# Kernel optimization log

Measured on AMD Instinct MI355X. Metric: run time of the kernel, lower is better.

## Reference

```python
import jax, jax.numpy as jnp
import numpy as np

VOCAB, HIDDEN, EMBED = 30522, 768, 512
PAD_INDEX = 0
NEG_SLOPE = 0.1


def setup_inputs() -> dict:
    key = jax.random.key(0)
    k1, k2, k3, k4 = jax.random.split(key, 4)
    words = jax.random.randint(k1, (16, 512, 4), 0, VOCAB, dtype=jnp.int64) if jax.config.jax_enable_x64 else jax.random.randint(k1, (16, 512, 4), 0, VOCAB, dtype=jnp.int32)
    embed_table = jax.random.normal(k2, (VOCAB, HIDDEN), dtype=jnp.float32) * 0.02
    w_ffn = jax.random.normal(k3, (HIDDEN, EMBED), dtype=jnp.float32) * 0.02
    b_ffn = jax.random.normal(k4, (EMBED,), dtype=jnp.float32) * 0.02
    return {"words": words, "embed_table": embed_table, "w_ffn": w_ffn, "b_ffn": b_ffn}


def reference(words, embed_table, w_ffn, b_ffn):
    # words: [B, S, W] subword ids; pad_index marks padding subwords/words.
    B, S, W = words.shape
    sub_mask = words != PAD_INDEX                      # [B,S,W] valid subwords
    word_valid = jnp.any(sub_mask, axis=-1)            # [B,S]  words with >=1 subword
    lens = jnp.sum(word_valid, axis=-1)                # [B]    valid words per sequence

    # Stub of transformer last_hidden_state: per-token hidden vectors. [B,S,W,H]
    x = embed_table[words]

    # Masked mean over subwords of each word (segment mean-pool).
    m = sub_mask[..., None].astype(x.dtype)
    cnt = jnp.maximum(jnp.sum(sub_mask, axis=-1), 1)[..., None].astype(x.dtype)
    pooled = jnp.sum(x * m, axis=2) / cnt              # [B,S,H]

    # pad = x[0, -1] of flattened [B, S*W, H] == hidden of last flat token of batch 0
    pad_vec = x[0, -1, -1]                             # [H]

    # Stable compaction: valid words first (mirrors pop-in-order + pad append).
    order = jnp.argsort(jnp.logical_not(word_valid), axis=1, stable=True)  # [B,S]
    pooled_c = jnp.take_along_axis(pooled, order[..., None], axis=1)       # [B,S,H]
    keep = (jnp.arange(S)[None, :] < lens[:, None])[..., None]             # [B,S,1]
    x_seq = jnp.where(keep, pooled_c, pad_vec)         # [B,S,H]

    # FFN: Linear + LeakyReLU(0.1)
    return jax.nn.leaky_relu(x_seq @ w_ffn + b_ffn, NEG_SLOPE)
```

## Files before the change

### kernel.cpp

```cpp
#include <hip/hip_runtime.h>
#include <stdint.h>

#define HIDDEN 768
#define EMBED  512
#define BATCH  16
#define SEQ    512
#define NWORDS (BATCH*SEQ)
#define PAD_FLAT_IDX 2047
#define NEG_SLOPE 0.1f

__device__ __forceinline__ unsigned short f2bf(float f) {
    unsigned int x = __float_as_uint(f);
    unsigned int r = x + 0x7fffu + ((x >> 16) & 1u);
    return (unsigned short)(r >> 16);
}

__global__ __launch_bounds__(512) void scan_kernel(const int* __restrict__ words,
                                                   int* __restrict__ dest) {
    int b = blockIdx.x;
    int s = threadIdx.x;
    int idx = b * SEQ + s;
    int4 w4 = ((const int4*)words)[idx];
    bool valid = (w4.x | w4.y | w4.z | w4.w) != 0;

    unsigned long long m = __ballot(valid);
    int lane = s & 63;
    int wave = s >> 6;
    int wpre = __popcll(m & ((1ull << lane) - 1ull));
    __shared__ int wsum[8];
    if (lane == 0) wsum[wave] = __popcll(m);
    __syncthreads();
    int off = 0, tot = 0;
#pragma unroll
    for (int i = 0; i < 8; ++i) {
        int t = wsum[i];
        if (i < wave) off += t;
        tot += t;
    }
    int vp = off + wpre;
    int d = valid ? vp : (tot + (s - vp));
    dest[idx] = b * SEQ + d;
}

__global__ __launch_bounds__(192) void pool_kernel(const int* __restrict__ words,
                                                   const float* __restrict__ table,
                                                   const int* __restrict__ dest,
                                                   unsigned short* __restrict__ xseq) {
    int word = blockIdx.x;
    int t = threadIdx.x;
    int4 w4 = ((const int4*)words)[word];
    int cnt = (w4.x != 0) + (w4.y != 0) + (w4.z != 0) + (w4.w != 0);

    float ax = 0.f, ay = 0.f, az = 0.f, aw = 0.f;
    if (cnt == 0) {
        int pid = words[PAD_FLAT_IDX];
        float4 v = ((const float4*)(table + (size_t)pid * HIDDEN))[t];
        ax = v.x; ay = v.y; az = v.z; aw = v.w;
    } else {
        if (w4.x != 0) { float4 v = ((const float4*)(table + (size_t)w4.x * HIDDEN))[t]; ax += v.x; ay += v.y; az += v.z; aw += v.w; }
        if (w4.y != 0) { float4 v = ((const float4*)(table + (size_t)w4.y * HIDDEN))[t]; ax += v.x; ay += v.y; az += v.z; aw += v.w; }
        if (w4.z != 0) { float4 v = ((const float4*)(table + (size_t)w4.z * HIDDEN))[t]; ax += v.x; ay += v.y; az += v.z; aw += v.w; }
        if (w4.w != 0) { float4 v = ((const float4*)(table + (size_t)w4.w * HIDDEN))[t]; ax += v.x; ay += v.y; az += v.z; aw += v.w; }
        float inv = 1.0f / (float)cnt;
        ax *= inv; ay *= inv; az *= inv; aw *= inv;
    }
    ushort4 o;
    o.x = f2bf(ax); o.y = f2bf(ay); o.z = f2bf(az); o.w = f2bf(aw);
    int drow = dest[word];
    ((ushort4*)(xseq + (size_t)drow * HIDDEN))[t] = o;
}

__global__ __launch_bounds__(256) void wt_kernel(const float* __restrict__ w,
                                                 unsigned short* __restrict__ wt) {
    __shared__ float tile[32][33];
    int k0 = blockIdx.x * 32;
    int n0 = blockIdx.y * 32;
    int tc = threadIdx.x & 31;
    int tr = threadIdx.x >> 5;
#pragma unroll
    for (int i = 0; i < 4; ++i) {
        int r = tr + i * 8;
        tile[r][tc] = w[(size_t)(k0 + r) * EMBED + n0 + tc];
    }
    __syncthreads();
#pragma unroll
    for (int i = 0; i < 4; ++i) {
        int r = tr + i * 8;
        wt[(size_t)(n0 + r) * HIDDEN + k0 + tc] = f2bf(tile[tc][r]);
    }
}

typedef __attribute__((ext_vector_type(8))) short bf16x8;
typedef __attribute__((ext_vector_type(4))) float f32x4;

__device__ __forceinline__ void load_lds16(const void* g, void* l) {
    __builtin_amdgcn_global_load_lds(
        (const __attribute__((address_space(1))) unsigned int*)g,
        (__attribute__((address_space(3))) unsigned int*)l,
        16, 0, 0);
}

#define BM 64
#define BN 128
#define BK 32

__global__ __launch_bounds__(256) void gemm_kernel(const unsigned short* __restrict__ A,
                                                   const unsigned short* __restrict__ Bt,
                                                   const float* __restrict__ bias,
                                                   float* __restrict__ out) {
    __shared__ unsigned short sA[BM * BK];
    __shared__ unsigned short sB[BN * BK];

    int tid  = threadIdx.x;
    int m0   = blockIdx.x * BM;
    int n0   = blockIdx.y * BN;
    int wave = tid >> 6;
    int lane = tid & 63;
    int wr   = wave >> 1;
    int wc   = wave & 1;
    int quad = lane >> 4;
    int l16  = lane & 15;

    f32x4 acc[2][4] = {};

    int r_s = tid >> 2;
    int k_s = (tid & 3) * 8;

    const unsigned short* ga = A  + (size_t)(m0 + r_s) * HIDDEN + k_s;
    const unsigned short* gb0 = Bt + (size_t)(n0 + r_s) * HIDDEN + k_s;
    const unsigned short* gb1 = Bt + (size_t)(n0 + r_s + 64) * HIDDEN + k_s;

    for (int k0 = 0; k0 < HIDDEN; k0 += BK) {
        load_lds16(ga + k0,  &sA[tid * 8]);
        load_lds16(gb0 + k0, &sB[tid * 8]);
        load_lds16(gb1 + k0, &sB[(256 + tid) * 8]);
        __syncthreads();

        bf16x8 af[2], bf[4];
#pragma unroll
        for (int mt = 0; mt < 2; ++mt)
            af[mt] = *(const bf16x8*)&sA[(wr * 32 + mt * 16 + l16) * BK + quad * 8];
#pragma unroll
        for (int nt = 0; nt < 4; ++nt)
            bf[nt] = *(const bf16x8*)&sB[(wc * 64 + nt * 16 + l16) * BK + quad * 8];

#pragma unroll
        for (int mt = 0; mt < 2; ++mt)
#pragma unroll
            for (int nt = 0; nt < 4; ++nt)
                acc[mt][nt] = __builtin_amdgcn_mfma_f32_16x16x32_bf16(
                    af[mt], bf[nt], acc[mt][nt], 0, 0, 0);
        __syncthreads();
    }

#pragma unroll
    for (int nt = 0; nt < 4; ++nt) {
        int col = n0 + wc * 64 + nt * 16 + l16;
        float bv = bias[col];
#pragma unroll
        for (int mt = 0; mt < 2; ++mt) {
            int rbase = m0 + wr * 32 + mt * 16 + quad * 4;
#pragma unroll
            for (int r = 0; r < 4; ++r) {
                float v = acc[mt][nt][r] + bv;
                v = (v > 0.f) ? v : v * NEG_SLOPE;
                out[(size_t)(rbase + r) * EMBED + col] = v;
            }
        }
    }
}

extern "C" void kernel_launch(void* const* d_in, const int* in_sizes, int n_in,
                              void* d_out, int out_size, void* d_ws, size_t ws_size,
                              hipStream_t stream) {
    (void)in_sizes; (void)n_in; (void)out_size; (void)ws_size;
    const int*   words = (const int*)d_in[0];
    const float* table = (const float*)d_in[1];
    const float* wffn  = (const float*)d_in[2];
    const float* bffn  = (const float*)d_in[3];
    float* out = (float*)d_out;

    char* ws = (char*)d_ws;
    unsigned short* xseq = (unsigned short*)ws;
    unsigned short* wt   = (unsigned short*)(ws + 12582912);
    int*            dest = (int*)(ws + 12582912 + 786432);

    scan_kernel<<<BATCH, SEQ, 0, stream>>>(words, dest);
    wt_kernel<<<dim3(HIDDEN / 32, EMBED / 32), 256, 0, stream>>>(wffn, wt);
    pool_kernel<<<NWORDS, 192, 0, stream>>>(words, table, dest, xseq);
    gemm_kernel<<<dim3(NWORDS / BM, EMBED / BN), 256, 0, stream>>>(xseq, wt, bffn, out);
}
```

Baseline: 165.6 us.

## Merge scan and weight-transpose kernels, reshape GEMM tile to 128x64

Measured after the change: 162.5 us. About the same (-1.9%).

```diff
diff --git a/kernel.cpp b/kernel.cpp
--- a/kernel.cpp
+++ b/kernel.cpp
@@ -15,31 +15,60 @@
     return (unsigned short)(r >> 16);
 }
 
-__global__ __launch_bounds__(512) void scan_kernel(const int* __restrict__ words,
-                                                   int* __restrict__ dest) {
-    int b = blockIdx.x;
-    int s = threadIdx.x;
-    int idx = b * SEQ + s;
-    int4 w4 = ((const int4*)words)[idx];
-    bool valid = (w4.x | w4.y | w4.z | w4.w) != 0;
+__global__ __launch_bounds__(256) void prep_kernel(const int* __restrict__ words,
+                                                   const float* __restrict__ w,
+                                                   int* __restrict__ dest,
+                                                   unsigned short* __restrict__ wt) {
+    if (blockIdx.x < BATCH) {
+        int b = blockIdx.x;
+        int t = threadIdx.x;
+        int s0 = 2 * t, s1 = 2 * t + 1;
+        int4 wa = ((const int4*)words)[b * SEQ + s0];
+        int4 wb = ((const int4*)words)[b * SEQ + s1];
+        bool v0 = (wa.x | wa.y | wa.z | wa.w) != 0;
+        bool v1 = (wb.x | wb.y | wb.z | wb.w) != 0;
 
-    unsigned long long m = __ballot(valid);
-    int lane = s & 63;
-    int wave = s >> 6;
-    int wpre = __popcll(m & ((1ull << lane) - 1ull));
-    __shared__ int wsum[8];
-    if (lane == 0) wsum[wave] = __popcll(m);
-    __syncthreads();
-    int off = 0, tot = 0;
+        unsigned long long m0 = __ballot(v0);
+        unsigned long long m1 = __ballot(v1);
+        int lane = t & 63;
+        int wave = t >> 6;
+        unsigned long long below = (1ull << lane) - 1ull;
+        int pre = __popcll(m0 & below) + __popcll(m1 & below);
+        __shared__ int wsum[4];
+        if (lane == 0) wsum[wave] = __popcll(m0) + __popcll(m1);
+        __syncthreads();
+        int off = 0, tot = 0;
 #pragma unroll
-    for (int i = 0; i < 8; ++i) {
-        int t = wsum[i];
-        if (i < wave) off += t;
-        tot += t;
+        for (int i = 0; i < 4; ++i) {
+            int x = wsum[i];
+            if (i < wave) off += x;
+            tot += x;
+        }
+        int vp0 = off + pre;
+        int vp1 = vp0 + (v0 ? 1 : 0);
+        int d0 = v0 ? vp0 : (tot + (s0 - vp0));
+        int d1 = v1 ? vp1 : (tot + (s1 - vp1));
+        dest[b * SEQ + s0] = b * SEQ + d0;
+        dest[b * SEQ + s1] = b * SEQ + d1;
+    } else {
+        __shared__ float tile[32][33];
+        int bid = blockIdx.x - BATCH;
+        int k0 = (bid % (HIDDEN / 32)) * 32;
+        int n0 = (bid / (HIDDEN / 32)) * 32;
+        int tc = threadIdx.x & 31;
+        int tr = threadIdx.x >> 5;
+#pragma unroll
+        for (int i = 0; i < 4; ++i) {
+            int r = tr + i * 8;
+            tile[r][tc] = w[(size_t)(k0 + r) * EMBED + n0 + tc];
+        }
+        __syncthreads();
+#pragma unroll
+        for (int i = 0; i < 4; ++i) {
+            int r = tr + i * 8;
+            wt[(size_t)(n0 + r) * HIDDEN + k0 + tc] = f2bf(tile[tc][r]);
+        }
     }
-    int vp = off + wpre;
-    int d = valid ? vp : (tot + (s - vp));
-    dest[idx] = b * SEQ + d;
 }
 
 __global__ __launch_bounds__(192) void pool_kernel(const int* __restrict__ words,
@@ -48,6 +77,7 @@
                                                    unsigned short* __restrict__ xseq) {
     int word = blockIdx.x;
     int t = threadIdx.x;
+    int drow = dest[word];
     int4 w4 = ((const int4*)words)[word];
     int cnt = (w4.x != 0) + (w4.y != 0) + (w4.z != 0) + (w4.w != 0);
 
@@ -66,28 +96,7 @@
     }
     ushort4 o;
     o.x = f2bf(ax); o.y = f2bf(ay); o.z = f2bf(az); o.w = f2bf(aw);
-    int drow = dest[word];
     ((ushort4*)(xseq + (size_t)drow * HIDDEN))[t] = o;
-}
-
-__global__ __launch_bounds__(256) void wt_kernel(const float* __restrict__ w,
-                                                 unsigned short* __restrict__ wt) {
-    __shared__ float tile[32][33];
-    int k0 = blockIdx.x * 32;
-    int n0 = blockIdx.y * 32;
-    int tc = threadIdx.x & 31;
-    int tr = threadIdx.x >> 5;
-#pragma unroll
-    for (int i = 0; i < 4; ++i) {
-        int r = tr + i * 8;
-        tile[r][tc] = w[(size_t)(k0 + r) * EMBED + n0 + tc];
-    }
-    __syncthreads();
-#pragma unroll
-    for (int i = 0; i < 4; ++i) {
-        int r = tr + i * 8;
-        wt[(size_t)(n0 + r) * HIDDEN + k0 + tc] = f2bf(tile[tc][r]);
-    }
 }
 
 typedef __attribute__((ext_vector_type(8))) short bf16x8;
@@ -100,8 +109,8 @@
         16, 0, 0);
 }
 
-#define BM 64
-#define BN 128
+#define BM 128
+#define BN 64
 #define BK 32
 
 __global__ __launch_bounds__(256) void gemm_kernel(const unsigned short* __restrict__ A,
@@ -121,45 +130,42 @@
     int quad = lane >> 4;
     int l16  = lane & 15;
 
-    f32x4 acc[2][4] = {};
+    f32x4 acc[4][2] = {};
 
-    int r_s = tid >> 2;
-    int k_s = (tid & 3) * 8;
-
-    const unsigned short* ga = A  + (size_t)(m0 + r_s) * HIDDEN + k_s;
-    const unsigned short* gb0 = Bt + (size_t)(n0 + r_s) * HIDDEN + k_s;
-    const unsigned short* gb1 = Bt + (size_t)(n0 + r_s + 64) * HIDDEN + k_s;
+    const unsigned short* ga0 = A  + (size_t)(m0 + (tid >> 2)) * HIDDEN + (tid & 3) * 8;
+    const unsigned short* ga1 = A  + (size_t)(m0 + 64 + (tid >> 2)) * HIDDEN + (tid & 3) * 8;
+    const unsigned short* gb  = Bt + (size_t)(n0 + (tid >> 2)) * HIDDEN + (tid & 3) * 8;
 
     for (int k0 = 0; k0 < HIDDEN; k0 += BK) {
-        load_lds16(ga + k0,  &sA[tid * 8]);
-        load_lds16(gb0 + k0, &sB[tid * 8]);
-        load_lds16(gb1 + k0, &sB[(256 + tid) * 8]);
+        load_lds16(ga0 + k0, &sA[tid * 8]);
+        load_lds16(ga1 + k0, &sA[(256 + tid) * 8]);
+        load_lds16(gb  + k0, &sB[tid * 8]);
         __syncthreads();
 
-        bf16x8 af[2], bf[4];
+        bf16x8 af[4], bf[2];
 #pragma unroll
-        for (int mt = 0; mt < 2; ++mt)
-            af[mt] = *(const bf16x8*)&sA[(wr * 32 + mt * 16 + l16) * BK + quad * 8];
+        for (int mt = 0; mt < 4; ++mt)
+            af[mt] = *(const bf16x8*)&sA[(wr * 64 + mt * 16 + l16) * BK + quad * 8];
 #pragma unroll
-        for (int nt = 0; nt < 4; ++nt)
-            bf[nt] = *(const bf16x8*)&sB[(wc * 64 + nt * 16 + l16) * BK + quad * 8];
+        for (int nt = 0; nt < 2; ++nt)
+            bf[nt] = *(const bf16x8*)&sB[(wc * 32 + nt * 16 + l16) * BK + quad * 8];
 
 #pragma unroll
-        for (int mt = 0; mt < 2; ++mt)
+        for (int mt = 0; mt < 4; ++mt)
 #pragma unroll
-            for (int nt = 0; nt < 4; ++nt)
+            for (int nt = 0; nt < 2; ++nt)
                 acc[mt][nt] = __builtin_amdgcn_mfma_f32_16x16x32_bf16(
                     af[mt], bf[nt], acc[mt][nt], 0, 0, 0);
         __syncthreads();
     }
 
 #pragma unroll
-    for (int nt = 0; nt < 4; ++nt) {
-        int col = n0 + wc * 64 + nt * 16 + l16;
+    for (int nt = 0; nt < 2; ++nt) {
+        int col = n0 + wc * 32 + nt * 16 + l16;
         float bv = bias[col];
 #pragma unroll
-        for (int mt = 0; mt < 2; ++mt) {
-            int rbase = m0 + wr * 32 + mt * 16 + quad * 4;
+        for (int mt = 0; mt < 4; ++mt) {
+            int rbase = m0 + wr * 64 + mt * 16 + quad * 4;
 #pragma unroll
             for (int r = 0; r < 4; ++r) {
                 float v = acc[mt][nt][r] + bv;
@@ -185,8 +191,7 @@
     unsigned short* wt   = (unsigned short*)(ws + 12582912);
     int*            dest = (int*)(ws + 12582912 + 786432);
 
-    scan_kernel<<<BATCH, SEQ, 0, stream>>>(words, dest);
-    wt_kernel<<<dim3(HIDDEN / 32, EMBED / 32), 256, 0, stream>>>(wffn, wt);
+    prep_kernel<<<BATCH + (HIDDEN / 32) * (EMBED / 32), 256, 0, stream>>>(words, wffn, dest, wt);
     pool_kernel<<<NWORDS, 192, 0, stream>>>(words, table, dest, xseq);
     gemm_kernel<<<dim3(NWORDS / BM, EMBED / BN), 256, 0, stream>>>(xseq, wt, bffn, out);
 }
```
